# Optimization experiments

Hardware: AMD Instinct MI355X
Metric: run time of the kernel (lower is better)

Reference implementation:

```python
import jax, jax.numpy as jnp
import numpy as np

N = 100000      # nodes
E = 1600000     # edges
G = 1000        # graphs
F_IN, H, C = 9, 128, 2
BN_EPS = 1e-5


def setup_inputs() -> dict:
    key = jax.random.key(0)
    ks = jax.random.split(key, 12)
    inp = {}
    inp['x'] = jax.random.normal(ks[0], (N, F_IN), dtype=jnp.float32)
    inp['edge_index'] = jax.random.randint(ks[1], (2, E), 0, N, dtype=jnp.int32).astype(jnp.int64)
    # 1000 graphs of 100 contiguous nodes each (sorted batch vector, all graphs non-empty)
    inp['batch'] = (jnp.arange(N, dtype=jnp.int64) // (N // G))
    inp['W1'] = jax.random.normal(ks[2], (F_IN, H), dtype=jnp.float32) * 0.1
    inp['b1'] = jnp.zeros((H,), jnp.float32)
    inp['W2'] = jax.random.normal(ks[3], (H, H), dtype=jnp.float32) * 0.1
    inp['b2'] = jnp.zeros((H,), jnp.float32)
    inp['W3'] = jax.random.normal(ks[4], (H, H), dtype=jnp.float32) * 0.1
    inp['b3'] = jnp.zeros((H,), jnp.float32)
    for i in range(1, 4):
        inp[f'g{i}'] = jnp.ones((H,), jnp.float32)
        inp[f'be{i}'] = jnp.zeros((H,), jnp.float32)
        inp[f'rm{i}'] = jnp.zeros((H,), jnp.float32)
        inp[f'rv{i}'] = jnp.ones((H,), jnp.float32)
    inp['fw1'] = jax.random.normal(ks[5], (2 * H, H), dtype=jnp.float32) * 0.1
    inp['fb1'] = jnp.zeros((H,), jnp.float32)
    inp['fw2'] = jax.random.normal(ks[6], (H, H // 2), dtype=jnp.float32) * 0.1
    inp['fb2'] = jnp.zeros((H // 2,), jnp.float32)
    inp['fw3'] = jax.random.normal(ks[7], (H // 2, C), dtype=jnp.float32) * 0.1
    inp['fb3'] = jnp.zeros((C,), jnp.float32)
    return inp


def gcn_conv(x, W, b, src, dst):
    # PyG GCNConv: add self-loops, symmetric normalization D^-1/2 (A+I) D^-1/2, linear, bias
    loop = jnp.arange(N, dtype=src.dtype)
    s = jnp.concatenate([src, loop])
    d = jnp.concatenate([dst, loop])
    deg = jax.ops.segment_sum(jnp.ones_like(d, dtype=x.dtype), d, num_segments=N)
    dinv = jnp.where(deg > 0, jax.lax.rsqrt(deg), 0.0)
    norm = dinv[s] * dinv[d]                       # [E+N]
    h = x @ W                                       # [N,H]
    msg = h[s] * norm[:, None]                      # [E+N,H]  (dominant intermediate)
    out = jax.ops.segment_sum(msg, d, num_segments=N)
    return out + b


def bn_eval(x, g, be, rm, rv):
    return (x - rm) * jax.lax.rsqrt(rv + BN_EPS) * g + be


def reference(x, edge_index, batch, W1, b1, W2, b2, W3, b3,
              g1, be1, g2, be2, g3, be3, rm1, rv1, rm2, rv2, rm3, rv3,
              fw1, fb1, fw2, fb2, fw3, fb3):
    src, dst = edge_index[0], edge_index[1]
    h = jax.nn.relu(bn_eval(gcn_conv(x, W1, b1, src, dst), g1, be1, rm1, rv1))
    h = jax.nn.relu(bn_eval(gcn_conv(h, W2, b2, src, dst), g2, be2, rm2, rv2))
    h = jax.nn.relu(bn_eval(gcn_conv(h, W3, b3, src, dst), g3, be3, rm3, rv3))
    # global mean / max pool by graph id
    cnt = jax.ops.segment_sum(jnp.ones((N,), h.dtype), batch, num_segments=G)
    mean = jax.ops.segment_sum(h, batch, num_segments=G) / jnp.maximum(cnt, 1.0)[:, None]
    mx = jax.ops.segment_max(h, batch, num_segments=G)
    z = jnp.concatenate([mean, mx], axis=1)         # [G, 2H]
    z = jax.nn.relu(z @ fw1 + fb1)
    z = jax.nn.relu(z @ fw2 + fb2)
    return z @ fw3 + fb3                            # [G, C]
```

## Files before the change

kernel.cpp:

```cpp
#include <hip/hip_runtime.h>
#include <hip/hip_fp16.h>

#define N_NODES 100000
#define N_EDGES 1600000
#define N_GRAPHS 1000
#define FD_IN 9
#define FD_PAD 16
#define HDIM 128
#define NPG 100
#define BN_EPS 1e-5f
#define SCAN_CHUNK 1024

__global__ void k_hist_pe(const int* __restrict__ dst, int* __restrict__ cnt,
                          int* __restrict__ pe) {
    int i = blockIdx.x * blockDim.x + threadIdx.x;
    if (i < N_EDGES) pe[i] = atomicAdd(&cnt[dst[i]], 1);
}

__global__ void k_block_scan(const int* __restrict__ cnt, int* __restrict__ rowptr,
                             int* __restrict__ partials, float* __restrict__ dinv) {
    __shared__ int sums[256];
    int t = threadIdx.x;
    int idx = blockIdx.x * SCAN_CHUNK + t * 4;
    int v0 = 0, v1 = 0, v2 = 0, v3 = 0;
    if (idx + 3 < N_NODES) {
        int4 c = *(const int4*)&cnt[idx];
        v0 = c.x; v1 = c.y; v2 = c.z; v3 = c.w;
    } else {
        if (idx + 0 < N_NODES) v0 = cnt[idx + 0];
        if (idx + 1 < N_NODES) v1 = cnt[idx + 1];
        if (idx + 2 < N_NODES) v2 = cnt[idx + 2];
        if (idx + 3 < N_NODES) v3 = cnt[idx + 3];
    }
    int s = v0 + v1 + v2 + v3;
    sums[t] = s;
    __syncthreads();
    for (int off = 1; off < 256; off <<= 1) {
        int val = (t >= off) ? sums[t - off] : 0;
        __syncthreads();
        sums[t] += val;
        __syncthreads();
    }
    int excl = sums[t] - s;
    if (t == 255) partials[blockIdx.x] = sums[255];
    if (idx + 0 < N_NODES) { rowptr[idx + 0] = excl;                dinv[idx + 0] = rsqrtf((float)v0 + 1.0f); }
    if (idx + 1 < N_NODES) { rowptr[idx + 1] = excl + v0;           dinv[idx + 1] = rsqrtf((float)v1 + 1.0f); }
    if (idx + 2 < N_NODES) { rowptr[idx + 2] = excl + v0 + v1;      dinv[idx + 2] = rsqrtf((float)v2 + 1.0f); }
    if (idx + 3 < N_NODES) { rowptr[idx + 3] = excl + v0 + v1 + v2; dinv[idx + 3] = rsqrtf((float)v3 + 1.0f); }
}

__global__ void k_partial_scan(int* __restrict__ partials, int nb) {
    __shared__ int s[256];
    int t = threadIdx.x;
    int mine = (t < nb) ? partials[t] : 0;
    s[t] = mine;
    __syncthreads();
    for (int off = 1; off < 256; off <<= 1) {
        int val = (t >= off) ? s[t - off] : 0;
        __syncthreads();
        s[t] += val;
        __syncthreads();
    }
    if (t < nb) partials[t] = s[t] - mine;
    if (t == nb - 1) partials[nb] = s[t];
}

__global__ void k_add_offsets(int* __restrict__ rowptr, const int* __restrict__ partials,
                              int nb) {
    int i = blockIdx.x * blockDim.x + threadIdx.x;
    if (i < N_NODES) rowptr[i] = rowptr[i] + partials[i >> 10];
    if (i == 0) rowptr[N_NODES] = partials[nb];
}

__global__ void k_scatter(const int* __restrict__ src, const int* __restrict__ dst,
                          const int* __restrict__ rowptr, const int* __restrict__ pe,
                          int* __restrict__ col) {
    int e = blockIdx.x * blockDim.x + threadIdx.x;
    if (e < N_EDGES) col[rowptr[dst[e]] + pe[e]] = src[e];
}

__global__ __launch_bounds__(256) void k_scale_x(const float* __restrict__ x,
                                                 const float* __restrict__ dinv,
                                                 float* __restrict__ xs) {
    int i = blockIdx.x * blockDim.x + threadIdx.x;
    int v = i >> 4, k = i & 15;
    float val = (k < FD_IN) ? dinv[v] * x[v * FD_IN + k] : 0.f;
    xs[i] = val;
}

__global__ __launch_bounds__(256) void k_agg9(const float* __restrict__ xs,
                                              const int* __restrict__ rowptr,
                                              const int* __restrict__ col,
                                              const float* __restrict__ dinv,
                                              float* __restrict__ aggx) {
    int t = threadIdx.x;
    int v = blockIdx.x * 16 + (t >> 4);
    int f = t & 15;
    float acc = xs[v * FD_PAD + f];
    int r0 = rowptr[v], r1 = rowptr[v + 1];
    int i = r0;
    for (; i + 4 <= r1; i += 4) {
        int s0 = col[i], s1 = col[i + 1], s2 = col[i + 2], s3 = col[i + 3];
        float a0 = xs[s0 * FD_PAD + f];
        float a1 = xs[s1 * FD_PAD + f];
        float a2 = xs[s2 * FD_PAD + f];
        float a3 = xs[s3 * FD_PAD + f];
        acc += (a0 + a1) + (a2 + a3);
    }
    for (; i < r1; ++i) acc += xs[col[i] * FD_PAD + f];
    aggx[v * FD_PAD + f] = acc * dinv[v];
}

__device__ __forceinline__ float4 h4f(uint2 u) {
    __half2 h0 = *reinterpret_cast<__half2*>(&u.x);
    __half2 h1 = *reinterpret_cast<__half2*>(&u.y);
    float2 f0 = __half22float2(h0);
    float2 f1 = __half22float2(h1);
    return make_float4(f0.x, f0.y, f1.x, f1.y);
}

__global__ __launch_bounds__(256) void k_l1_gemm(const float* __restrict__ aggx,
                                                 const float* __restrict__ W1,
                                                 const float* __restrict__ b1,
                                                 const float* __restrict__ bn_g,
                                                 const float* __restrict__ bn_b,
                                                 const float* __restrict__ bn_rm,
                                                 const float* __restrict__ bn_rv,
                                                 const float* __restrict__ W2,
                                                 const float* __restrict__ dinv,
                                                 __half2* __restrict__ gh) {
    __shared__ float hs[32 * HDIM];
    __shared__ float w1s[FD_IN * HDIM];
    __shared__ float axs[32 * FD_PAD];
    int t = threadIdx.x;
    int node0 = blockIdx.x * 32;
    for (int i = t; i < FD_IN * HDIM; i += 256) w1s[i] = W1[i];
    for (int i = t; i < 32 * FD_PAD; i += 256) axs[i] = aggx[(size_t)node0 * FD_PAD + i];
    __syncthreads();
    {
        int f = t & 127, vh = t >> 7;
        float sc = bn_g[f] * rsqrtf(bn_rv[f] + BN_EPS);
        float bbf = bn_b[f], rmf = bn_rm[f], b1f = b1[f];
#pragma unroll
        for (int i = 0; i < 16; i++) {
            int vl = vh + 2 * i;
            float acc = b1f;
#pragma unroll
            for (int k = 0; k < FD_IN; k++) acc = fmaf(axs[vl * FD_PAD + k], w1s[k * HDIM + f], acc);
            hs[vl * HDIM + f] = fmaxf((acc - rmf) * sc + bbf, 0.f);
        }
    }
    __syncthreads();
    int f0 = (t & 63) * 2;
    int grp = t >> 6;
    float acc[8][2];
#pragma unroll
    for (int i = 0; i < 8; i++) { acc[i][0] = 0.f; acc[i][1] = 0.f; }
    for (int k = 0; k < HDIM; k += 4) {
        const float2 w0 = *(const float2*)&W2[(k + 0) * HDIM + f0];
        const float2 w1 = *(const float2*)&W2[(k + 1) * HDIM + f0];
        const float2 w2 = *(const float2*)&W2[(k + 2) * HDIM + f0];
        const float2 w3 = *(const float2*)&W2[(k + 3) * HDIM + f0];
#pragma unroll
        for (int i = 0; i < 8; i++) {
            const float4 hv = *(const float4*)&hs[(grp * 8 + i) * HDIM + k];
            acc[i][0] = fmaf(hv.x, w0.x, acc[i][0]); acc[i][1] = fmaf(hv.x, w0.y, acc[i][1]);
            acc[i][0] = fmaf(hv.y, w1.x, acc[i][0]); acc[i][1] = fmaf(hv.y, w1.y, acc[i][1]);
            acc[i][0] = fmaf(hv.z, w2.x, acc[i][0]); acc[i][1] = fmaf(hv.z, w2.y, acc[i][1]);
            acc[i][0] = fmaf(hv.w, w3.x, acc[i][0]); acc[i][1] = fmaf(hv.w, w3.y, acc[i][1]);
        }
    }
#pragma unroll
    for (int i = 0; i < 8; i++) {
        int v = node0 + grp * 8 + i;
        float dv = dinv[v];
        float2 o; o.x = acc[i][0] * dv; o.y = acc[i][1] * dv;
        gh[(size_t)v * 64 + (f0 >> 1)] = __float22half2_rn(o);
    }
}

__global__ __launch_bounds__(256) void k_gemm128(const float* __restrict__ h,
                                                 const float* __restrict__ W,
                                                 const float* __restrict__ dinv,
                                                 __half2* __restrict__ gh) {
    __shared__ float hs[32 * HDIM];
    int t = threadIdx.x;
    int node0 = blockIdx.x * 32;
    for (int i = t * 4; i < 32 * HDIM; i += 1024)
        *(float4*)&hs[i] = *(const float4*)&h[(size_t)node0 * HDIM + i];
    __syncthreads();
    int f0 = (t & 63) * 2;
    int grp = t >> 6;
    float acc[8][2];
#pragma unroll
    for (int i = 0; i < 8; i++) { acc[i][0] = 0.f; acc[i][1] = 0.f; }
    for (int k = 0; k < HDIM; k += 4) {
        const float2 w0 = *(const float2*)&W[(k + 0) * HDIM + f0];
        const float2 w1 = *(const float2*)&W[(k + 1) * HDIM + f0];
        const float2 w2 = *(const float2*)&W[(k + 2) * HDIM + f0];
        const float2 w3 = *(const float2*)&W[(k + 3) * HDIM + f0];
#pragma unroll
        for (int i = 0; i < 8; i++) {
            const float4 hv = *(const float4*)&hs[(grp * 8 + i) * HDIM + k];
            acc[i][0] = fmaf(hv.x, w0.x, acc[i][0]); acc[i][1] = fmaf(hv.x, w0.y, acc[i][1]);
            acc[i][0] = fmaf(hv.y, w1.x, acc[i][0]); acc[i][1] = fmaf(hv.y, w1.y, acc[i][1]);
            acc[i][0] = fmaf(hv.z, w2.x, acc[i][0]); acc[i][1] = fmaf(hv.z, w2.y, acc[i][1]);
            acc[i][0] = fmaf(hv.w, w3.x, acc[i][0]); acc[i][1] = fmaf(hv.w, w3.y, acc[i][1]);
        }
    }
#pragma unroll
    for (int i = 0; i < 8; i++) {
        int v = node0 + grp * 8 + i;
        float dv = dinv[v];
        float2 o; o.x = acc[i][0] * dv; o.y = acc[i][1] * dv;
        gh[(size_t)v * 64 + (f0 >> 1)] = __float22half2_rn(o);
    }
}

__global__ __launch_bounds__(256) void k_aggh(const uint2* __restrict__ g,
                                              const int* __restrict__ rowptr,
                                              const int* __restrict__ col,
                                              const float* __restrict__ dinv,
                                              const float* __restrict__ bias,
                                              const float* __restrict__ bn_g,
                                              const float* __restrict__ bn_b,
                                              const float* __restrict__ bn_rm,
                                              const float* __restrict__ bn_rv,
                                              float* __restrict__ out) {
    int t = threadIdx.x;
    int v = blockIdx.x * 8 + (t >> 5);
    int q = t & 31;
    int f = q * 4;
    float4 acc, acc2;
    {
        float4 s = h4f(g[(size_t)v * 32 + q]);
        acc = s;
        acc2 = make_float4(0.f, 0.f, 0.f, 0.f);
    }
    int r0 = rowptr[v], r1 = rowptr[v + 1];
    int i = r0;
    for (; i + 8 <= r1; i += 8) {
        int s0 = col[i],     s1 = col[i + 1], s2 = col[i + 2], s3 = col[i + 3];
        int s4 = col[i + 4], s5 = col[i + 5], s6 = col[i + 6], s7 = col[i + 7];
        uint2 u0 = g[(size_t)s0 * 32 + q];
        uint2 u1 = g[(size_t)s1 * 32 + q];
        uint2 u2 = g[(size_t)s2 * 32 + q];
        uint2 u3 = g[(size_t)s3 * 32 + q];
        uint2 u4 = g[(size_t)s4 * 32 + q];
        uint2 u5 = g[(size_t)s5 * 32 + q];
        uint2 u6 = g[(size_t)s6 * 32 + q];
        uint2 u7 = g[(size_t)s7 * 32 + q];
        float4 a0 = h4f(u0), a1 = h4f(u1), a2 = h4f(u2), a3 = h4f(u3);
        float4 a4 = h4f(u4), a5 = h4f(u5), a6 = h4f(u6), a7 = h4f(u7);
        acc.x  += (a0.x + a1.x) + (a2.x + a3.x);
        acc.y  += (a0.y + a1.y) + (a2.y + a3.y);
        acc.z  += (a0.z + a1.z) + (a2.z + a3.z);
        acc.w  += (a0.w + a1.w) + (a2.w + a3.w);
        acc2.x += (a4.x + a5.x) + (a6.x + a7.x);
        acc2.y += (a4.y + a5.y) + (a6.y + a7.y);
        acc2.z += (a4.z + a5.z) + (a6.z + a7.z);
        acc2.w += (a4.w + a5.w) + (a6.w + a7.w);
    }
    if (i + 4 <= r1) {
        int s0 = col[i], s1 = col[i + 1], s2 = col[i + 2], s3 = col[i + 3];
        uint2 u0 = g[(size_t)s0 * 32 + q];
        uint2 u1 = g[(size_t)s1 * 32 + q];
        uint2 u2 = g[(size_t)s2 * 32 + q];
        uint2 u3 = g[(size_t)s3 * 32 + q];
        float4 a0 = h4f(u0), a1 = h4f(u1), a2 = h4f(u2), a3 = h4f(u3);
        acc.x += (a0.x + a1.x) + (a2.x + a3.x);
        acc.y += (a0.y + a1.y) + (a2.y + a3.y);
        acc.z += (a0.z + a1.z) + (a2.z + a3.z);
        acc.w += (a0.w + a1.w) + (a2.w + a3.w);
        i += 4;
    }
    for (; i < r1; ++i) {
        float4 a = h4f(g[(size_t)col[i] * 32 + q]);
        acc2.x += a.x; acc2.y += a.y; acc2.z += a.z; acc2.w += a.w;
    }
    acc.x += acc2.x; acc.y += acc2.y; acc.z += acc2.z; acc.w += acc2.w;
    float dv = dinv[v];
    const float4 bi = *(const float4*)&bias[f];
    const float4 bg = *(const float4*)&bn_g[f];
    const float4 bb = *(const float4*)&bn_b[f];
    const float4 rm = *(const float4*)&bn_rm[f];
    const float4 rv = *(const float4*)&bn_rv[f];
    float4 o;
    o.x = fmaxf((fmaf(acc.x, dv, bi.x) - rm.x) * (bg.x * rsqrtf(rv.x + BN_EPS)) + bb.x, 0.f);
    o.y = fmaxf((fmaf(acc.y, dv, bi.y) - rm.y) * (bg.y * rsqrtf(rv.y + BN_EPS)) + bb.y, 0.f);
    o.z = fmaxf((fmaf(acc.z, dv, bi.z) - rm.z) * (bg.z * rsqrtf(rv.z + BN_EPS)) + bb.z, 0.f);
    o.w = fmaxf((fmaf(acc.w, dv, bi.w) - rm.w) * (bg.w * rsqrtf(rv.w + BN_EPS)) + bb.w, 0.f);
    *(float4*)&out[(size_t)v * HDIM + f] = o;
}

__global__ __launch_bounds__(128) void k_pool_mlp(const float* __restrict__ h,
                                                  const float* __restrict__ fw1, const float* __restrict__ fb1,
                                                  const float* __restrict__ fw2, const float* __restrict__ fb2,
                                                  const float* __restrict__ fw3, const float* __restrict__ fb3,
                                                  float* __restrict__ out) {
    __shared__ float zm[HDIM], zx[HDIM], z1[HDIM], z2[64];
    int gr = blockIdx.x;
    int f = threadIdx.x;
    int base = gr * NPG;
    float sum = 0.f, mx = -INFINITY;
    for (int i = 0; i < NPG; i++) {
        float val = h[(size_t)(base + i) * HDIM + f];
        sum += val;
        mx = fmaxf(mx, val);
    }
    zm[f] = sum / (float)NPG;
    zx[f] = mx;
    __syncthreads();
    float acc = fb1[f];
    for (int k = 0; k < HDIM; k++) acc = fmaf(zm[k], fw1[k * HDIM + f], acc);
    for (int k = 0; k < HDIM; k++) acc = fmaf(zx[k], fw1[(HDIM + k) * HDIM + f], acc);
    z1[f] = fmaxf(acc, 0.f);
    __syncthreads();
    if (f < 64) {
        float a2 = fb2[f];
        for (int k = 0; k < HDIM; k++) a2 = fmaf(z1[k], fw2[k * 64 + f], a2);
        z2[f] = fmaxf(a2, 0.f);
    }
    __syncthreads();
    if (f < 2) {
        float a3 = fb3[f];
        for (int k = 0; k < 64; k++) a3 = fmaf(z2[k], fw3[k * 2 + f], a3);
        out[gr * 2 + f] = a3;
    }
}

extern "C" void kernel_launch(void* const* d_in, const int* in_sizes, int n_in,
                              void* d_out, int out_size, void* d_ws, size_t ws_size,
                              hipStream_t stream) {
    const float* x   = (const float*)d_in[0];
    const int*   ei  = (const int*)d_in[1];
    const float* W1  = (const float*)d_in[3];
    const float* b1  = (const float*)d_in[4];
    const float* W2  = (const float*)d_in[5];
    const float* b2  = (const float*)d_in[6];
    const float* W3  = (const float*)d_in[7];
    const float* b3  = (const float*)d_in[8];
    const float* g1  = (const float*)d_in[9];
    const float* be1 = (const float*)d_in[10];
    const float* rm1 = (const float*)d_in[11];
    const float* rv1 = (const float*)d_in[12];
    const float* g2  = (const float*)d_in[13];
    const float* be2 = (const float*)d_in[14];
    const float* rm2 = (const float*)d_in[15];
    const float* rv2 = (const float*)d_in[16];
    const float* g3  = (const float*)d_in[17];
    const float* be3 = (const float*)d_in[18];
    const float* rm3 = (const float*)d_in[19];
    const float* rv3 = (const float*)d_in[20];
    const float* fw1 = (const float*)d_in[21];
    const float* fb1 = (const float*)d_in[22];
    const float* fw2 = (const float*)d_in[23];
    const float* fb2 = (const float*)d_in[24];
    const float* fw3 = (const float*)d_in[25];
    const float* fb3 = (const float*)d_in[26];

    char* ws = (char*)d_ws;
    size_t off = 0;
    auto alloc = [&](size_t bytes) -> void* {
        void* p = ws + off;
        off += (bytes + 255) & ~(size_t)255;
        return p;
    };
    int*   cnt      = (int*)alloc((size_t)N_NODES * 4);
    int*   rowptr   = (int*)alloc(((size_t)N_NODES + 1) * 4);
    int*   partials = (int*)alloc(256 * 4);
    float* dinv     = (float*)alloc((size_t)N_NODES * 4);
    int*   col      = (int*)alloc((size_t)N_EDGES * 4);
    int*   pe       = (int*)alloc((size_t)N_EDGES * 4);
    float* bufA     = (float*)alloc((size_t)N_NODES * HDIM * 4);
    float* bufB     = (float*)alloc((size_t)N_NODES * HDIM * 4);
    float*   xs   = (float*)pe;
    float*   aggx = bufA;
    __half2* gh   = (__half2*)(bufA + (size_t)N_NODES * FD_PAD);

    const int* src = ei;
    const int* dst = ei + N_EDGES;

    hipMemsetAsync(cnt, 0, (size_t)N_NODES * 4, stream);
    k_hist_pe<<<(N_EDGES + 255) / 256, 256, 0, stream>>>(dst, cnt, pe);
    int nb = (N_NODES + SCAN_CHUNK - 1) / SCAN_CHUNK;
    k_block_scan<<<nb, 256, 0, stream>>>(cnt, rowptr, partials, dinv);
    k_partial_scan<<<1, 256, 0, stream>>>(partials, nb);
    k_add_offsets<<<(N_NODES + 255) / 256, 256, 0, stream>>>(rowptr, partials, nb);
    k_scatter<<<(N_EDGES + 255) / 256, 256, 0, stream>>>(src, dst, rowptr, pe, col);

    k_scale_x<<<(N_NODES * FD_PAD) / 256, 256, 0, stream>>>(x, dinv, xs);
    k_agg9<<<N_NODES / 16, 256, 0, stream>>>(xs, rowptr, col, dinv, aggx);
    k_l1_gemm<<<N_NODES / 32, 256, 0, stream>>>(aggx, W1, b1, g1, be1, rm1, rv1,
                                                W2, dinv, gh);
    k_aggh<<<N_NODES / 8, 256, 0, stream>>>((const uint2*)gh, rowptr, col, dinv, b2, g2, be2, rm2, rv2, bufB);
    k_gemm128<<<N_NODES / 32, 256, 0, stream>>>(bufB, W3, dinv, gh);
    k_aggh<<<N_NODES / 8, 256, 0, stream>>>((const uint2*)gh, rowptr, col, dinv, b3, g3, be3, rm3, rv3, bufB);
    k_pool_mlp<<<N_GRAPHS, 128, 0, stream>>>(bufB, fw1, fb1, fw2, fb2, fw3, fb3, (float*)d_out);
}
```

Baseline: 400.8 us.

## Replace random CSR column scatter with two-pass bucketed scatter through LDS

The single random scatter into the CSR column array is split into two passes. The first pass packs each edge's local offset and source into a 32-bit word and appends it to a 2048-slot bucket chosen by destination position, using a per-bucket atomic counter. The second pass has one block per bucket place the entries in LDS and write them back to col contiguously. The aim is to turn scattered 4-byte global writes into coalesced ones, at the cost of an extra kernel, a memset, per-bucket atomic contention and a round trip through a temporary buffer.

```diff
diff --git a/kernel.cpp b/kernel.cpp
--- a/kernel.cpp
+++ b/kernel.cpp
@@ -10,6 +10,9 @@
 #define NPG 100
 #define BN_EPS 1e-5f
 #define SCAN_CHUNK 1024
+#define BKT_SH 11
+#define BKT_SZ 2048
+#define NBKT ((N_EDGES + BKT_SZ - 1) / BKT_SZ)
 
 __global__ void k_hist_pe(const int* __restrict__ dst, int* __restrict__ cnt,
                           int* __restrict__ pe) {
@@ -72,11 +75,34 @@
     if (i == 0) rowptr[N_NODES] = partials[nb];
 }
 
-__global__ void k_scatter(const int* __restrict__ src, const int* __restrict__ dst,
-                          const int* __restrict__ rowptr, const int* __restrict__ pe,
-                          int* __restrict__ col) {
+__global__ __launch_bounds__(256) void k_scat1(const int* __restrict__ src,
+                                               const int* __restrict__ dst,
+                                               const int* __restrict__ rowptr,
+                                               const int* __restrict__ pe,
+                                               int* __restrict__ bwp,
+                                               unsigned* __restrict__ pairs) {
     int e = blockIdx.x * blockDim.x + threadIdx.x;
-    if (e < N_EDGES) col[rowptr[dst[e]] + pe[e]] = src[e];
+    if (e < N_EDGES) {
+        int p = rowptr[dst[e]] + pe[e];
+        int b = p >> BKT_SH;
+        int slot = atomicAdd(&bwp[b], 1);
+        pairs[((size_t)b << BKT_SH) + slot] = ((unsigned)(p & (BKT_SZ - 1)) << 17) | (unsigned)src[e];
+    }
+}
+
+__global__ __launch_bounds__(256) void k_scat2(const unsigned* __restrict__ pairs,
+                                               int* __restrict__ col) {
+    __shared__ int lds[BKT_SZ];
+    int b = blockIdx.x;
+    int base = b << BKT_SH;
+    int count = min(BKT_SZ, N_EDGES - base);
+    for (int i = threadIdx.x; i < count; i += 256) {
+        unsigned u = pairs[(size_t)base + i];
+        lds[u >> 17] = (int)(u & 0x1FFFFu);
+    }
+    __syncthreads();
+    for (int i = threadIdx.x; i < count; i += 256)
+        col[base + i] = lds[i];
 }
 
 __global__ __launch_bounds__(256) void k_scale_x(const float* __restrict__ x,
@@ -369,25 +395,29 @@
     int*   cnt      = (int*)alloc((size_t)N_NODES * 4);
     int*   rowptr   = (int*)alloc(((size_t)N_NODES + 1) * 4);
     int*   partials = (int*)alloc(256 * 4);
+    int*   bwp      = (int*)alloc((size_t)NBKT * 4);
     float* dinv     = (float*)alloc((size_t)N_NODES * 4);
     int*   col      = (int*)alloc((size_t)N_EDGES * 4);
     int*   pe       = (int*)alloc((size_t)N_EDGES * 4);
     float* bufA     = (float*)alloc((size_t)N_NODES * HDIM * 4);
     float* bufB     = (float*)alloc((size_t)N_NODES * HDIM * 4);
-    float*   xs   = (float*)pe;
-    float*   aggx = bufA;
-    __half2* gh   = (__half2*)(bufA + (size_t)N_NODES * FD_PAD);
+    unsigned* pairs = (unsigned*)bufB;
+    float*    xs   = (float*)pe;
+    float*    aggx = bufA;
+    __half2*  gh   = (__half2*)(bufA + (size_t)N_NODES * FD_PAD);
 
     const int* src = ei;
     const int* dst = ei + N_EDGES;
 
     hipMemsetAsync(cnt, 0, (size_t)N_NODES * 4, stream);
+    hipMemsetAsync(bwp, 0, (size_t)NBKT * 4, stream);
     k_hist_pe<<<(N_EDGES + 255) / 256, 256, 0, stream>>>(dst, cnt, pe);
     int nb = (N_NODES + SCAN_CHUNK - 1) / SCAN_CHUNK;
     k_block_scan<<<nb, 256, 0, stream>>>(cnt, rowptr, partials, dinv);
     k_partial_scan<<<1, 256, 0, stream>>>(partials, nb);
     k_add_offsets<<<(N_NODES + 255) / 256, 256, 0, stream>>>(rowptr, partials, nb);
-    k_scatter<<<(N_EDGES + 255) / 256, 256, 0, stream>>>(src, dst, rowptr, pe, col);
+    k_scat1<<<(N_EDGES + 255) / 256, 256, 0, stream>>>(src, dst, rowptr, pe, bwp, pairs);
+    k_scat2<<<NBKT, 256, 0, stream>>>(pairs, col);
 
     k_scale_x<<<(N_NODES * FD_PAD) / 256, 256, 0, stream>>>(x, dinv, xs);
     k_agg9<<<N_NODES / 16, 256, 0, stream>>>(xs, rowptr, col, dinv, aggx);
```

After: 767.0 us. 91.4% more time.

## Stage weight tiles in shared memory with 4x4 register-blocked GEMM

Applied to the files above, without the earlier changes.

The two 128-wide GEMM kernels switch from reading W straight from global memory (a float2 per thread per k) to loading 32-row chunks of W into LDS, then computing a 4-node by 4-feature register tile per thread. The shared GEMM body is factored into one device function used by both kernels. The goal is less global and L2 traffic per FMA and a higher FMA-to-load ratio. In exchange it adds 16KB of LDS per block, which can lower occupancy, and extra barriers for each K chunk.

```diff
diff --git a/kernel.cpp b/kernel.cpp
--- a/kernel.cpp
+++ b/kernel.cpp
@@ -119,6 +119,62 @@
     return make_float4(f0.x, f0.y, f1.x, f1.y);
 }
 
+__device__ __forceinline__ void gemm32_body(const float* hs, float* ws,
+                                            const float* __restrict__ W,
+                                            const float* __restrict__ dinv,
+                                            __half2* __restrict__ gh,
+                                            int node0, int t) {
+    int c4 = (t & 31) * 4;
+    int g  = t >> 5;
+    float4 a0 = make_float4(0.f, 0.f, 0.f, 0.f);
+    float4 a1 = a0, a2 = a0, a3 = a0;
+    for (int kc = 0; kc < HDIM; kc += 32) {
+        __syncthreads();
+        for (int i = t * 4; i < 32 * HDIM; i += 1024)
+            *(float4*)&ws[i] = *(const float4*)&W[kc * HDIM + i];
+        __syncthreads();
+#pragma unroll
+        for (int k = 0; k < 32; k += 4) {
+            const float4 w0 = *(const float4*)&ws[(k + 0) * HDIM + c4];
+            const float4 w1 = *(const float4*)&ws[(k + 1) * HDIM + c4];
+            const float4 w2 = *(const float4*)&ws[(k + 2) * HDIM + c4];
+            const float4 w3 = *(const float4*)&ws[(k + 3) * HDIM + c4];
+            const float4 h0 = *(const float4*)&hs[(g * 4 + 0) * HDIM + kc + k];
+            const float4 h1 = *(const float4*)&hs[(g * 4 + 1) * HDIM + kc + k];
+            const float4 h2 = *(const float4*)&hs[(g * 4 + 2) * HDIM + kc + k];
+            const float4 h3 = *(const float4*)&hs[(g * 4 + 3) * HDIM + kc + k];
+            a0.x = fmaf(h0.x, w0.x, a0.x); a0.y = fmaf(h0.x, w0.y, a0.y); a0.z = fmaf(h0.x, w0.z, a0.z); a0.w = fmaf(h0.x, w0.w, a0.w);
+            a0.x = fmaf(h0.y, w1.x, a0.x); a0.y = fmaf(h0.y, w1.y, a0.y); a0.z = fmaf(h0.y, w1.z, a0.z); a0.w = fmaf(h0.y, w1.w, a0.w);
+            a0.x = fmaf(h0.z, w2.x, a0.x); a0.y = fmaf(h0.z, w2.y, a0.y); a0.z = fmaf(h0.z, w2.z, a0.z); a0.w = fmaf(h0.z, w2.w, a0.w);
+            a0.x = fmaf(h0.w, w3.x, a0.x); a0.y = fmaf(h0.w, w3.y, a0.y); a0.z = fmaf(h0.w, w3.z, a0.z); a0.w = fmaf(h0.w, w3.w, a0.w);
+            a1.x = fmaf(h1.x, w0.x, a1.x); a1.y = fmaf(h1.x, w0.y, a1.y); a1.z = fmaf(h1.x, w0.z, a1.z); a1.w = fmaf(h1.x, w0.w, a1.w);
+            a1.x = fmaf(h1.y, w1.x, a1.x); a1.y = fmaf(h1.y, w1.y, a1.y); a1.z = fmaf(h1.y, w1.z, a1.z); a1.w = fmaf(h1.y, w1.w, a1.w);
+            a1.x = fmaf(h1.z, w2.x, a1.x); a1.y = fmaf(h1.z, w2.y, a1.y); a1.z = fmaf(h1.z, w2.z, a1.z); a1.w = fmaf(h1.z, w2.w, a1.w);
+            a1.x = fmaf(h1.w, w3.x, a1.x); a1.y = fmaf(h1.w, w3.y, a1.y); a1.z = fmaf(h1.w, w3.z, a1.z); a1.w = fmaf(h1.w, w3.w, a1.w);
+            a2.x = fmaf(h2.x, w0.x, a2.x); a2.y = fmaf(h2.x, w0.y, a2.y); a2.z = fmaf(h2.x, w0.z, a2.z); a2.w = fmaf(h2.x, w0.w, a2.w);
+            a2.x = fmaf(h2.y, w1.x, a2.x); a2.y = fmaf(h2.y, w1.y, a2.y); a2.z = fmaf(h2.y, w1.z, a2.z); a2.w = fmaf(h2.y, w1.w, a2.w);
+            a2.x = fmaf(h2.z, w2.x, a2.x); a2.y = fmaf(h2.z, w2.y, a2.y); a2.z = fmaf(h2.z, w2.z, a2.z); a2.w = fmaf(h2.z, w2.w, a2.w);
+            a2.x = fmaf(h2.w, w3.x, a2.x); a2.y = fmaf(h2.w, w3.y, a2.y); a2.z = fmaf(h2.w, w3.z, a2.z); a2.w = fmaf(h2.w, w3.w, a2.w);
+            a3.x = fmaf(h3.x, w0.x, a3.x); a3.y = fmaf(h3.x, w0.y, a3.y); a3.z = fmaf(h3.x, w0.z, a3.z); a3.w = fmaf(h3.x, w0.w, a3.w);
+            a3.x = fmaf(h3.y, w1.x, a3.x); a3.y = fmaf(h3.y, w1.y, a3.y); a3.z = fmaf(h3.y, w1.z, a3.z); a3.w = fmaf(h3.y, w1.w, a3.w);
+            a3.x = fmaf(h3.z, w2.x, a3.x); a3.y = fmaf(h3.z, w2.y, a3.y); a3.z = fmaf(h3.z, w2.z, a3.z); a3.w = fmaf(h3.z, w2.w, a3.w);
+            a3.x = fmaf(h3.w, w3.x, a3.x); a3.y = fmaf(h3.w, w3.y, a3.y); a3.z = fmaf(h3.w, w3.z, a3.z); a3.w = fmaf(h3.w, w3.w, a3.w);
+        }
+    }
+#pragma unroll
+    for (int n = 0; n < 4; n++) {
+        float4 a = (n == 0) ? a0 : (n == 1) ? a1 : (n == 2) ? a2 : a3;
+        int v = node0 + g * 4 + n;
+        float dv = dinv[v];
+        __half2 p0 = __float22half2_rn(make_float2(a.x * dv, a.y * dv));
+        __half2 p1 = __float22half2_rn(make_float2(a.z * dv, a.w * dv));
+        uint2 pk;
+        pk.x = *reinterpret_cast<unsigned*>(&p0);
+        pk.y = *reinterpret_cast<unsigned*>(&p1);
+        *(uint2*)&gh[(size_t)v * 64 + (c4 >> 1)] = pk;
+    }
+}
+
 __global__ __launch_bounds__(256) void k_l1_gemm(const float* __restrict__ aggx,
                                                  const float* __restrict__ W1,
                                                  const float* __restrict__ b1,
@@ -130,6 +186,7 @@
                                                  const float* __restrict__ dinv,
                                                  __half2* __restrict__ gh) {
     __shared__ float hs[32 * HDIM];
+    __shared__ float ws[32 * HDIM];
     __shared__ float w1s[FD_IN * HDIM];
     __shared__ float axs[32 * FD_PAD];
     int t = threadIdx.x;
@@ -150,33 +207,7 @@
             hs[vl * HDIM + f] = fmaxf((acc - rmf) * sc + bbf, 0.f);
         }
     }
-    __syncthreads();
-    int f0 = (t & 63) * 2;
-    int grp = t >> 6;
-    float acc[8][2];
-#pragma unroll
-    for (int i = 0; i < 8; i++) { acc[i][0] = 0.f; acc[i][1] = 0.f; }
-    for (int k = 0; k < HDIM; k += 4) {
-        const float2 w0 = *(const float2*)&W2[(k + 0) * HDIM + f0];
-        const float2 w1 = *(const float2*)&W2[(k + 1) * HDIM + f0];
-        const float2 w2 = *(const float2*)&W2[(k + 2) * HDIM + f0];
-        const float2 w3 = *(const float2*)&W2[(k + 3) * HDIM + f0];
-#pragma unroll
-        for (int i = 0; i < 8; i++) {
-            const float4 hv = *(const float4*)&hs[(grp * 8 + i) * HDIM + k];
-            acc[i][0] = fmaf(hv.x, w0.x, acc[i][0]); acc[i][1] = fmaf(hv.x, w0.y, acc[i][1]);
-            acc[i][0] = fmaf(hv.y, w1.x, acc[i][0]); acc[i][1] = fmaf(hv.y, w1.y, acc[i][1]);
-            acc[i][0] = fmaf(hv.z, w2.x, acc[i][0]); acc[i][1] = fmaf(hv.z, w2.y, acc[i][1]);
-            acc[i][0] = fmaf(hv.w, w3.x, acc[i][0]); acc[i][1] = fmaf(hv.w, w3.y, acc[i][1]);
-        }
-    }
-#pragma unroll
-    for (int i = 0; i < 8; i++) {
-        int v = node0 + grp * 8 + i;
-        float dv = dinv[v];
-        float2 o; o.x = acc[i][0] * dv; o.y = acc[i][1] * dv;
-        gh[(size_t)v * 64 + (f0 >> 1)] = __float22half2_rn(o);
-    }
+    gemm32_body(hs, ws, W2, dinv, gh, node0, t);
 }
 
 __global__ __launch_bounds__(256) void k_gemm128(const float* __restrict__ h,
@@ -184,37 +215,12 @@
                                                  const float* __restrict__ dinv,
                                                  __half2* __restrict__ gh) {
     __shared__ float hs[32 * HDIM];
+    __shared__ float ws[32 * HDIM];
     int t = threadIdx.x;
     int node0 = blockIdx.x * 32;
     for (int i = t * 4; i < 32 * HDIM; i += 1024)
         *(float4*)&hs[i] = *(const float4*)&h[(size_t)node0 * HDIM + i];
-    __syncthreads();
-    int f0 = (t & 63) * 2;
-    int grp = t >> 6;
-    float acc[8][2];
-#pragma unroll
-    for (int i = 0; i < 8; i++) { acc[i][0] = 0.f; acc[i][1] = 0.f; }
-    for (int k = 0; k < HDIM; k += 4) {
-        const float2 w0 = *(const float2*)&W[(k + 0) * HDIM + f0];
-        const float2 w1 = *(const float2*)&W[(k + 1) * HDIM + f0];
-        const float2 w2 = *(const float2*)&W[(k + 2) * HDIM + f0];
-        const float2 w3 = *(const float2*)&W[(k + 3) * HDIM + f0];
-#pragma unroll
-        for (int i = 0; i < 8; i++) {
-            const float4 hv = *(const float4*)&hs[(grp * 8 + i) * HDIM + k];
-            acc[i][0] = fmaf(hv.x, w0.x, acc[i][0]); acc[i][1] = fmaf(hv.x, w0.y, acc[i][1]);
-            acc[i][0] = fmaf(hv.y, w1.x, acc[i][0]); acc[i][1] = fmaf(hv.y, w1.y, acc[i][1]);
-            acc[i][0] = fmaf(hv.z, w2.x, acc[i][0]); acc[i][1] = fmaf(hv.z, w2.y, acc[i][1]);
-            acc[i][0] = fmaf(hv.w, w3.x, acc[i][0]); acc[i][1] = fmaf(hv.w, w3.y, acc[i][1]);
-        }
-    }
-#pragma unroll
-    for (int i = 0; i < 8; i++) {
-        int v = node0 + grp * 8 + i;
-        float dv = dinv[v];
-        float2 o; o.x = acc[i][0] * dv; o.y = acc[i][1] * dv;
-        gh[(size_t)v * 64 + (f0 >> 1)] = __float22half2_rn(o);
-    }
+    gemm32_body(hs, ws, W, dinv, gh, node0, t);
 }
 
 __global__ __launch_bounds__(256) void k_aggh(const uint2* __restrict__ g,
```

After: 390.4 us. 2.6% less time.
